# Kernel optimization log

Hardware: AMD Instinct MI355X
Metric: run time of the kernel (lower is better)

## Reference

```python
import jax, jax.numpy as jnp
import numpy as np

K = 3        # kernel_size
STRIDE = 1
PAD = 1
OUT_H = 64
OUT_W = 64


def _unfold(x):
    """torch.nn.Unfold equivalent: x (B,C,H,W) -> patches (B, L, C*K*K),
    feature index ordered c*K*K + ki*K + kj (channel-major, like torch)."""
    B, C, H, W = x.shape
    xp = jnp.pad(x, ((0, 0), (0, 0), (PAD, PAD), (PAD, PAD)))
    # gather K*K shifted views; loop is over the small fixed kernel window only
    rows = []
    for ki in range(K):
        cols = []
        for kj in range(K):
            cols.append(xp[:, :, ki:ki + STRIDE * OUT_H:STRIDE,
                               kj:kj + STRIDE * OUT_W:STRIDE])  # (B,C,oh,ow)
        rows.append(jnp.stack(cols, axis=2))  # (B,C,K,oh,ow)
    p = jnp.stack(rows, axis=2)               # (B,C,K,K,oh,ow)
    # -> (B, oh, ow, C, K, K) -> (B, L, C*K*K)
    p = p.transpose(0, 4, 5, 1, 2, 3)
    return p.reshape(B, OUT_H * OUT_W, C * K * K)


def setup_inputs() -> dict:
    key = jax.random.key(0)
    k1, k2, k3 = jax.random.split(key, 3)
    B, C = 16, 32
    out_ch = 64
    L = OUT_H * OUT_W                 # 4096
    in_feat = C * K * K               # 288
    x = jax.random.normal(k1, (B, C, 64, 64), dtype=jnp.float32)
    # kaiming_uniform with a=sqrt(5) on (in_feat, out_ch) slices -> bound = 1/sqrt(in_feat)
    bound = 1.0 / np.sqrt(in_feat)
    weight = jax.random.uniform(k2, (L, in_feat, out_ch), dtype=jnp.float32,
                                minval=-bound, maxval=bound)
    bias = jax.random.uniform(k3, (L, out_ch), dtype=jnp.float32,
                              minval=-bound, maxval=bound)
    return {"x": x, "weight": weight, "bias": bias}


def reference(x, weight, bias):
    B = x.shape[0]
    out_ch = weight.shape[-1]
    patches = _unfold(x)                               # (B, L, in_feat)
    out = jnp.einsum('bli,lio->blo', patches, weight)  # per-location matmul
    out = out + bias[None]                             # (B, L, out_ch)
    out = out.transpose(0, 2, 1).reshape(B, out_ch, OUT_H, OUT_W)
    return out
```

## Files before the change

### kernel.cpp

```cpp
#include <hip/hip_runtime.h>

#define L_TOT   4096
#define CIN     32
#define G_L     4
#define CH      4
#define NCHUNK  24
#define CHUNK_STRIDE_F (CH * 3 * 64)

using f32g = __attribute__((address_space(1))) const float;
using f32l = __attribute__((address_space(3))) float;

#define FMA16(PP, WW) {                                                        \
    acc[0][0] += PP.x * WW.x; acc[0][1] += PP.x * WW.y;                        \
    acc[0][2] += PP.x * WW.z; acc[0][3] += PP.x * WW.w;                        \
    acc[1][0] += PP.y * WW.x; acc[1][1] += PP.y * WW.y;                        \
    acc[1][2] += PP.y * WW.z; acc[1][3] += PP.y * WW.w;                        \
    acc[2][0] += PP.z * WW.x; acc[2][1] += PP.z * WW.y;                        \
    acc[2][2] += PP.z * WW.z; acc[2][3] += PP.z * WW.w;                        \
    acc[3][0] += PP.w * WW.x; acc[3][1] += PP.w * WW.y;                        \
    acc[3][2] += PP.w * WW.z; acc[3][3] += PP.w * WW.w; }

__global__ __launch_bounds__(256, 2)
void lc2d_v6(const float* __restrict__ x,
             const float* __restrict__ weight,
             const float* __restrict__ bias,
             float* __restrict__ out) {
    __shared__ __align__(16) float xs[576 * 16];
    __shared__ __align__(16) float wsm[2][12 * 256];

    const int tid  = threadIdx.x;
    const int lane = tid & 63;
    const int wv   = tid >> 6;
    const int g    = lane >> 4;
    const int o4   = lane & 15;
    const int l0   = blockIdx.x * G_L;
    const int oh   = l0 >> 6;
    const int ow0  = l0 & 63;

    const float* gsrc[3];
    int ldsoff[3];
#pragma unroll
    for (int t = 0; t < 3; ++t) {
        int p   = wv + (t << 2);
        int gg  = p / 3;
        int sub = p - 3 * gg;
        gsrc[t] = weight + (size_t)(l0 + gg) * (288 * 64) + sub * 256 + (lane << 2);
        ldsoff[t] = p * 256;
    }

#pragma unroll
    for (int t = 0; t < 3; ++t)
        __builtin_amdgcn_global_load_lds((f32g*)(gsrc[t]),
                                         (f32l*)(&wsm[0][ldsoff[t]]), 16, 0, 0);

    for (int u = tid; u < 1536; u += 256) {
        int b  = u & 15;
        int t  = u >> 4;
        int dh = t % 3;
        int c  = t / 3;
        int h  = oh - 1 + dh;
        bool hok = (unsigned)h < 64u;
        const float* xrow = x + (((b * CIN + c) * 64 + h) << 6);
        int wbase = ow0 - 1;
#pragma unroll
        for (int wl = 0; wl < 6; ++wl) {
            int ww = wbase + wl;
            float v = (hok && (unsigned)ww < 64u) ? xrow[ww] : 0.0f;
            xs[(t * 6 + wl) * 16 + b] = v;
        }
    }
    __syncthreads();

    const float4 bias4 = ((const float4*)bias)[(l0 + g) * 16 + o4];
    float acc[4][4];
#pragma unroll
    for (int bq = 0; bq < 4; ++bq) {
        acc[bq][0] = bias4.x; acc[bq][1] = bias4.y;
        acc[bq][2] = bias4.z; acc[bq][3] = bias4.w;
    }

    int buf = 0;
    for (int k = 0; k < NCHUNK - 1; ++k) {
#pragma unroll
        for (int t = 0; t < 3; ++t)
            __builtin_amdgcn_global_load_lds((f32g*)(gsrc[t] + (size_t)(k + 1) * CHUNK_STRIDE_F),
                                             (f32l*)(&wsm[buf ^ 1][ldsoff[t]]), 16, 0, 0);
#pragma unroll
        for (int sl = 0; sl < CH; ++sl) {
            const int s = (k << 2) + sl;
            const float* pr = xs + ((6 * s + g) << 4) + (wv << 2);
            float4 p0 = *(const float4*)(pr);
            float4 p1 = *(const float4*)(pr + 16);
            float4 p2 = *(const float4*)(pr + 32);
            const float4* wr = (const float4*)&wsm[buf][0] + g * 192 + sl * 48 + o4;
            float4 w0 = wr[0];
            float4 w1 = wr[16];
            float4 w2 = wr[32];
            FMA16(p0, w0); FMA16(p1, w1); FMA16(p2, w2);
        }
        __syncthreads();
        buf ^= 1;
    }
#pragma unroll
    for (int sl = 0; sl < CH; ++sl) {
        const int s = ((NCHUNK - 1) << 2) + sl;
        const float* pr = xs + ((6 * s + g) << 4) + (wv << 2);
        float4 p0 = *(const float4*)(pr);
        float4 p1 = *(const float4*)(pr + 16);
        float4 p2 = *(const float4*)(pr + 32);
        const float4* wr = (const float4*)&wsm[buf][0] + g * 192 + sl * 48 + o4;
        float4 w0 = wr[0];
        float4 w1 = wr[16];
        float4 w2 = wr[32];
        FMA16(p0, w0); FMA16(p1, w1); FMA16(p2, w2);
    }

#pragma unroll
    for (int bq = 0; bq < 4; ++bq) {
        const int b = (wv << 2) + bq;
#pragma unroll
        for (int j = 0; j < 4; ++j) {
            out[((size_t)((b << 6) + (o4 << 2) + j) << 12) + l0 + g] = acc[bq][j];
        }
    }
}

extern "C" void kernel_launch(void* const* d_in, const int* in_sizes, int n_in,
                              void* d_out, int out_size, void* d_ws, size_t ws_size,
                              hipStream_t stream) {
    const float* x      = (const float*)d_in[0];
    const float* weight = (const float*)d_in[1];
    const float* bias   = (const float*)d_in[2];
    float* out          = (float*)d_out;

    dim3 grid(L_TOT / G_L);
    dim3 block(256);
    hipLaunchKernelGGL(lc2d_v6, grid, block, 0, stream, x, weight, bias, out);
}
```

Before: 444.2 us.

## Triple-buffer weight staging with partial vmcnt waits and swizzle block order

Moves the weight streaming from a double buffer to a triple buffer so that two chunks are in flight ahead of compute. The full __syncthreads is replaced by an explicit s_waitcnt vmcnt(3) plus a barrier, so the next chunk's async loads can stay outstanding. Block indices are also swizzled across spatial rows, which changes how the x-patch and output accesses spread across CUs and caches. The cost is more LDS per block, which may limit occupancy, and the waitcnt values are hand-tuned and could break if the compiler reorders memory ops.

```diff
diff --git a/kernel.cpp b/kernel.cpp
--- a/kernel.cpp
+++ b/kernel.cpp
@@ -20,20 +20,39 @@
     acc[3][0] += PP.w * WW.x; acc[3][1] += PP.w * WW.y;                        \
     acc[3][2] += PP.w * WW.z; acc[3][3] += PP.w * WW.w; }
 
+#define COMPUTE4(K, WOFF) {                                                    \
+    _Pragma("unroll")                                                          \
+    for (int sl = 0; sl < CH; ++sl) {                                          \
+        const int s = ((K) << 2) + sl;                                         \
+        const float* pr = xs + ((6 * s + g) << 4) + (wv << 2);                 \
+        float4 p0 = *(const float4*)(pr);                                      \
+        float4 p1 = *(const float4*)(pr + 16);                                 \
+        float4 p2 = *(const float4*)(pr + 32);                                 \
+        const float4* wr = (const float4*)(&wsm[0][0] + (WOFF))                \
+                           + g * 192 + sl * 48 + o4;                           \
+        float4 w0 = wr[0];                                                     \
+        float4 w1 = wr[16];                                                    \
+        float4 w2 = wr[32];                                                    \
+        FMA16(p0, w0); FMA16(p1, w1); FMA16(p2, w2);                           \
+    } }
+
 __global__ __launch_bounds__(256, 2)
-void lc2d_v6(const float* __restrict__ x,
+void lc2d_v7(const float* __restrict__ x,
              const float* __restrict__ weight,
              const float* __restrict__ bias,
              float* __restrict__ out) {
     __shared__ __align__(16) float xs[576 * 16];
-    __shared__ __align__(16) float wsm[2][12 * 256];
+    __shared__ __align__(16) float wsm[3][12 * 256];
 
     const int tid  = threadIdx.x;
     const int lane = tid & 63;
     const int wv   = tid >> 6;
     const int g    = lane >> 4;
     const int o4   = lane & 15;
-    const int l0   = blockIdx.x * G_L;
+
+    const int bid  = blockIdx.x;
+    const int swz  = ((bid & 7) << 7) | (bid >> 3);
+    const int l0   = swz * G_L;
     const int oh   = l0 >> 6;
     const int ow0  = l0 & 63;
 
@@ -52,6 +71,10 @@
     for (int t = 0; t < 3; ++t)
         __builtin_amdgcn_global_load_lds((f32g*)(gsrc[t]),
                                          (f32l*)(&wsm[0][ldsoff[t]]), 16, 0, 0);
+#pragma unroll
+    for (int t = 0; t < 3; ++t)
+        __builtin_amdgcn_global_load_lds((f32g*)(gsrc[t] + CHUNK_STRIDE_F),
+                                         (f32l*)(&wsm[1][ldsoff[t]]), 16, 0, 0);
 
     for (int u = tid; u < 1536; u += 256) {
         int b  = u & 15;
@@ -79,41 +102,26 @@
         acc[bq][2] = bias4.z; acc[bq][3] = bias4.w;
     }
 
-    int buf = 0;
-    for (int k = 0; k < NCHUNK - 1; ++k) {
+    int wo0 = 0;
+    int wo1 = 12 * 256;
+    int wo2 = 2 * 12 * 256;
+    for (int k = 0; k < NCHUNK - 2; ++k) {
 #pragma unroll
         for (int t = 0; t < 3; ++t)
-            __builtin_amdgcn_global_load_lds((f32g*)(gsrc[t] + (size_t)(k + 1) * CHUNK_STRIDE_F),
-                                             (f32l*)(&wsm[buf ^ 1][ldsoff[t]]), 16, 0, 0);
-#pragma unroll
-        for (int sl = 0; sl < CH; ++sl) {
-            const int s = (k << 2) + sl;
-            const float* pr = xs + ((6 * s + g) << 4) + (wv << 2);
-            float4 p0 = *(const float4*)(pr);
-            float4 p1 = *(const float4*)(pr + 16);
-            float4 p2 = *(const float4*)(pr + 32);
-            const float4* wr = (const float4*)&wsm[buf][0] + g * 192 + sl * 48 + o4;
-            float4 w0 = wr[0];
-            float4 w1 = wr[16];
-            float4 w2 = wr[32];
-            FMA16(p0, w0); FMA16(p1, w1); FMA16(p2, w2);
-        }
-        __syncthreads();
-        buf ^= 1;
+            __builtin_amdgcn_global_load_lds(
+                (f32g*)(gsrc[t] + (size_t)(k + 2) * CHUNK_STRIDE_F),
+                (f32l*)(&wsm[0][0] + wo2 + ldsoff[t]), 16, 0, 0);
+        COMPUTE4(k, wo0);
+        asm volatile("s_waitcnt vmcnt(3) lgkmcnt(0)" ::: "memory");
+        __builtin_amdgcn_s_barrier();
+        asm volatile("" ::: "memory");
+        int tmp = wo0; wo0 = wo1; wo1 = wo2; wo2 = tmp;
     }
-#pragma unroll
-    for (int sl = 0; sl < CH; ++sl) {
-        const int s = ((NCHUNK - 1) << 2) + sl;
-        const float* pr = xs + ((6 * s + g) << 4) + (wv << 2);
-        float4 p0 = *(const float4*)(pr);
-        float4 p1 = *(const float4*)(pr + 16);
-        float4 p2 = *(const float4*)(pr + 32);
-        const float4* wr = (const float4*)&wsm[buf][0] + g * 192 + sl * 48 + o4;
-        float4 w0 = wr[0];
-        float4 w1 = wr[16];
-        float4 w2 = wr[32];
-        FMA16(p0, w0); FMA16(p1, w1); FMA16(p2, w2);
-    }
+    COMPUTE4(NCHUNK - 2, wo0);
+    asm volatile("s_waitcnt vmcnt(0) lgkmcnt(0)" ::: "memory");
+    __builtin_amdgcn_s_barrier();
+    asm volatile("" ::: "memory");
+    COMPUTE4(NCHUNK - 1, wo1);
 
 #pragma unroll
     for (int bq = 0; bq < 4; ++bq) {
@@ -135,5 +143,5 @@
 
     dim3 grid(L_TOT / G_L);
     dim3 block(256);
-    hipLaunchKernelGGL(lc2d_v6, grid, block, 0, stream, x, weight, bias, out);
+    hipLaunchKernelGGL(lc2d_v7, grid, block, 0, stream, x, weight, bias, out);
 }
```

Result: no change. 442.9 us (-0.3%).
